# Kernel tuning notes

Measured on AMD Instinct MI355X. Metric: run time of the kernel, lower is better.

The kernel has to match this reference:

```python
import jax, jax.numpy as jnp
import numpy as np

QMIN, QMAX = -128, 127
EPS = float(np.finfo(np.float32).eps)


def _choose_qparams_and_quantize(x):
    # per-token asymmetric int8 qparams (token = all dims but last)
    mn = jnp.min(x, axis=-1, keepdims=True)
    mx = jnp.max(x, axis=-1, keepdims=True)
    mn = jnp.minimum(mn, 0.0)
    mx = jnp.maximum(mx, 0.0)
    scale = jnp.maximum((mx - mn) / float(QMAX - QMIN), EPS)
    d_min = mn / scale
    d_max = mx / scale
    zp = jnp.where((QMIN + d_min) + (QMAX + d_max) > 0, QMIN - d_min, QMAX - d_max)
    zp = jnp.round(jnp.clip(zp, QMIN, QMAX))
    q = jnp.clip(jnp.round(x / scale) + zp, QMIN, QMAX).astype(jnp.int8)
    return q, scale, zp.astype(jnp.int64)


def _dequant(q, scale, zp):
    return (q.astype(jnp.float32) - zp.astype(jnp.float32)) * scale


def setup_inputs() -> dict:
    key = jax.random.key(0)
    k1, k2 = jax.random.split(key)
    B, S, H, D = 1, 8192, 32, 128
    Snew = 128
    return {
        "input_pos": jnp.arange(Snew, dtype=jnp.int64),
        "k_val": jax.random.normal(k1, (B, Snew, H, D), dtype=jnp.float32),
        "v_val": jax.random.normal(k2, (B, Snew, H, D), dtype=jnp.float32),
        "k_cache": jnp.zeros((B, S, H, D), dtype=jnp.int8),
        "v_cache": jnp.zeros((B, S, H, D), dtype=jnp.int8),
        "k_cache_scales": jnp.ones((B, S, H, 1), dtype=jnp.float32),
        "v_cache_scales": jnp.ones((B, S, H, 1), dtype=jnp.float32),
        "k_cache_zero_points": jnp.ones((B, S, H, 1), dtype=jnp.int64),
        "v_cache_zero_points": jnp.ones((B, S, H, 1), dtype=jnp.int64),
    }


def reference(input_pos, k_val, v_val, k_cache, v_cache,
              k_cache_scales, v_cache_scales,
              k_cache_zero_points, v_cache_zero_points):
    qk, ks, kzp = _choose_qparams_and_quantize(k_val)
    qv, vs, vzp = _choose_qparams_and_quantize(v_val)
    start = input_pos[0]
    zero = jnp.zeros((), dtype=start.dtype)
    idx = (zero, start, zero, zero)
    k_cache = jax.lax.dynamic_update_slice(k_cache, qk, idx)
    k_cache_scales = jax.lax.dynamic_update_slice(k_cache_scales, ks, idx)
    k_cache_zero_points = jax.lax.dynamic_update_slice(k_cache_zero_points, kzp, idx)
    v_cache = jax.lax.dynamic_update_slice(v_cache, qv, idx)
    v_cache_scales = jax.lax.dynamic_update_slice(v_cache_scales, vs, idx)
    v_cache_zero_points = jax.lax.dynamic_update_slice(v_cache_zero_points, vzp, idx)
    k_out = _dequant(k_cache, k_cache_scales, k_cache_zero_points)
    v_out = _dequant(v_cache, v_cache_scales, v_cache_zero_points)
    return (k_out, v_out)
```

## Files before the change

kernel.cpp:

```cpp
#include <hip/hip_runtime.h>

constexpr int S = 8192, Snew = 128, H = 32, D = 128;
constexpr float QMINf = -128.0f, QMAXf = 127.0f;
constexpr float EPSf = 1.1920928955078125e-07f;

__global__ __launch_bounds__(256) void quant_update(
    const float* __restrict__ k_val, const float* __restrict__ v_val,
    const int* __restrict__ input_pos, float* __restrict__ out)
{
    const int gid  = blockIdx.x * 256 + threadIdx.x;
    const int wave = gid >> 6;
    const int lane = gid & 63;
    constexpr int TOK = Snew * H;
    if (wave >= 2 * TOK) return;
    const int tensor = wave >= TOK;
    const int tok    = tensor ? wave - TOK : wave;
    const float* src = tensor ? v_val : k_val;

    long long start = input_pos[0];
    if (start < 0) start = 0;
    if (start > (long long)(S - Snew)) start = S - Snew;

    const float2 x = ((const float2*)(src + (size_t)tok * D))[lane];
    float mn = fminf(x.x, x.y), mx = fmaxf(x.x, x.y);
    #pragma unroll
    for (int off = 1; off < 64; off <<= 1) {
        mn = fminf(mn, __shfl_xor(mn, off, 64));
        mx = fmaxf(mx, __shfl_xor(mx, off, 64));
    }
    mn = fminf(mn, 0.0f);
    mx = fmaxf(mx, 0.0f);
    const float scale = fmaxf((mx - mn) / 255.0f, EPSf);
    const float dmin = mn / scale;
    const float dmax = mx / scale;
    float zp = ((QMINf + dmin) + (QMAXf + dmax) > 0.0f) ? (QMINf - dmin)
                                                        : (QMAXf - dmax);
    zp = rintf(fminf(fmaxf(zp, QMINf), QMAXf));

    const float q0 = fminf(fmaxf(rintf(x.x / scale) + zp, QMINf), QMAXf);
    const float q1 = fminf(fmaxf(rintf(x.y / scale) + zp, QMINf), QMAXf);
    const float2 o = make_float2((q0 - zp) * scale, (q1 - zp) * scale);

    const int s_new = tok >> 5;
    const int h     = tok & (H - 1);
    const size_t off_el =
        ((size_t)tensor * S * H + (size_t)(start + s_new) * H + h) * (size_t)D;
    ((float2*)(out + off_el))[lane] = o;
}

__global__ __launch_bounds__(256) void dequant_cache(
    const int* __restrict__ k_cache, const int* __restrict__ v_cache,
    const float* __restrict__ k_scales, const float* __restrict__ v_scales,
    const int* __restrict__ k_zp, const int* __restrict__ v_zp,
    const int* __restrict__ input_pos, float* __restrict__ out)
{
    constexpr size_t TOK    = (size_t)S * H;
    constexpr size_t GROUPS = TOK * (D / 4);
    constexpr size_t TOTAL  = 2 * GROUPS;

    long long start = input_pos[0];
    if (start < 0) start = 0;
    if (start > (long long)(S - Snew)) start = S - Snew;
    const size_t s_lo = (size_t)start, s_hi = (size_t)start + Snew;

    const size_t stride = (size_t)gridDim.x * blockDim.x;
    for (size_t i = (size_t)blockIdx.x * blockDim.x + threadIdx.x;
         i < TOTAL; i += stride) {
        const size_t token  = i >> 5;
        const int    tensor = token >= TOK;
        const size_t tt     = tensor ? token - TOK : token;
        const size_t s      = tt >> 5;
        if (s >= s_lo && s < s_hi) continue;
        const size_t ig = tensor ? i - GROUPS : i;

        const int4  q4    = ((const int4*)(tensor ? v_cache : k_cache))[ig];
        const float scale = (tensor ? v_scales : k_scales)[tt];
        const float zp    = (float)(tensor ? v_zp : k_zp)[tt];

        float4 o;
        o.x = ((float)q4.x - zp) * scale;
        o.y = ((float)q4.y - zp) * scale;
        o.z = ((float)q4.z - zp) * scale;
        o.w = ((float)q4.w - zp) * scale;
        ((float4*)out)[i] = o;
    }
}

extern "C" void kernel_launch(void* const* d_in, const int* in_sizes, int n_in,
                              void* d_out, int out_size, void* d_ws, size_t ws_size,
                              hipStream_t stream) {
    (void)in_sizes; (void)n_in; (void)out_size; (void)d_ws; (void)ws_size;
    const int*   input_pos = (const int*)d_in[0];
    const float* k_val     = (const float*)d_in[1];
    const float* v_val     = (const float*)d_in[2];
    const int*   k_cache   = (const int*)d_in[3];
    const int*   v_cache   = (const int*)d_in[4];
    const float* k_scales  = (const float*)d_in[5];
    const float* v_scales  = (const float*)d_in[6];
    const int*   k_zp      = (const int*)d_in[7];
    const int*   v_zp      = (const int*)d_in[8];
    float*       out       = (float*)d_out;

    dequant_cache<<<2048, 256, 0, stream>>>(k_cache, v_cache,
                                            k_scales, v_scales,
                                            k_zp, v_zp, input_pos, out);
    quant_update<<<(2 * Snew * H * 64) / 256, 256, 0, stream>>>(
        k_val, v_val, input_pos, out);
}
```

Before: 113.9 us.

## Fuse quantize-update and cache dequant into one kernel with nontemporal accesses

Merges the two launches into one kernel: each block first quantizes four new tokens for its tensor, then runs a fixed-trip, unrolled grid-stride dequant loop over the cache with 32-bit indexing and nontemporal loads and stores. The goal is to remove a kernel launch and its serialization, cut 64-bit index arithmetic, and keep streaming data out of the caches. In exchange, every cache group is now loaded even inside the overwritten window (only the store is masked), and correctness depends on the two parts writing disjoint regions of the output.

```diff
diff --git a/kernel.cpp b/kernel.cpp
--- a/kernel.cpp
+++ b/kernel.cpp
@@ -1,88 +1,85 @@
 #include <hip/hip_runtime.h>
 
 constexpr int S = 8192, Snew = 128, H = 32, D = 128;
+constexpr int TOKENS = S * H;
+constexpr int GROUPS = TOKENS * (D / 4);
+constexpr int BLOCKS_HALF = 1024;
+constexpr int THREADS_HALF = BLOCKS_HALF * 256;
+constexpr int ITERS = GROUPS / THREADS_HALF;
+constexpr int GROUPS_PER_S = H * (D / 4);
 constexpr float QMINf = -128.0f, QMAXf = 127.0f;
 constexpr float EPSf = 1.1920928955078125e-07f;
 
-__global__ __launch_bounds__(256) void quant_update(
+typedef int   i32x4 __attribute__((ext_vector_type(4)));
+typedef float f32x4 __attribute__((ext_vector_type(4)));
+
+__global__ __launch_bounds__(256) void fused_kv(
     const float* __restrict__ k_val, const float* __restrict__ v_val,
+    const int* __restrict__ k_cache, const int* __restrict__ v_cache,
+    const float* __restrict__ k_scales, const float* __restrict__ v_scales,
+    const int* __restrict__ k_zp, const int* __restrict__ v_zp,
     const int* __restrict__ input_pos, float* __restrict__ out)
 {
-    const int gid  = blockIdx.x * 256 + threadIdx.x;
-    const int wave = gid >> 6;
-    const int lane = gid & 63;
-    constexpr int TOK = Snew * H;
-    if (wave >= 2 * TOK) return;
-    const int tensor = wave >= TOK;
-    const int tok    = tensor ? wave - TOK : wave;
-    const float* src = tensor ? v_val : k_val;
+    const int b      = blockIdx.x;
+    const int tensor = (b >= BLOCKS_HALF);
+    const int bh     = tensor ? b - BLOCKS_HALF : b;
 
     long long start = input_pos[0];
     if (start < 0) start = 0;
     if (start > (long long)(S - Snew)) start = S - Snew;
 
-    const float2 x = ((const float2*)(src + (size_t)tok * D))[lane];
-    float mn = fminf(x.x, x.y), mx = fmaxf(x.x, x.y);
-    #pragma unroll
-    for (int off = 1; off < 64; off <<= 1) {
-        mn = fminf(mn, __shfl_xor(mn, off, 64));
-        mx = fmaxf(mx, __shfl_xor(mx, off, 64));
+    {
+        const int lane = threadIdx.x & 63;
+        const int wv   = threadIdx.x >> 6;
+        const int tok  = bh * 4 + wv;
+        const float* src = tensor ? v_val : k_val;
+        const float2 x = ((const float2*)(src + (size_t)tok * D))[lane];
+        float mn = fminf(x.x, x.y), mx = fmaxf(x.x, x.y);
+        #pragma unroll
+        for (int off = 1; off < 64; off <<= 1) {
+            mn = fminf(mn, __shfl_xor(mn, off, 64));
+            mx = fmaxf(mx, __shfl_xor(mx, off, 64));
+        }
+        mn = fminf(mn, 0.0f);
+        mx = fmaxf(mx, 0.0f);
+        const float scale = fmaxf((mx - mn) / 255.0f, EPSf);
+        const float dmin = mn / scale, dmax = mx / scale;
+        float zp = ((QMINf + dmin) + (QMAXf + dmax) > 0.0f) ? (QMINf - dmin)
+                                                            : (QMAXf - dmax);
+        zp = rintf(fminf(fmaxf(zp, QMINf), QMAXf));
+        const float q0 = fminf(fmaxf(rintf(x.x / scale) + zp, QMINf), QMAXf);
+        const float q1 = fminf(fmaxf(rintf(x.y / scale) + zp, QMINf), QMAXf);
+        const int s_new = tok >> 5;
+        const int h     = tok & (H - 1);
+        const size_t off_el =
+            ((size_t)tensor * TOKENS + (size_t)(start + s_new) * H + h) * (size_t)D;
+        ((float2*)(out + off_el))[lane] =
+            make_float2((q0 - zp) * scale, (q1 - zp) * scale);
     }
-    mn = fminf(mn, 0.0f);
-    mx = fmaxf(mx, 0.0f);
-    const float scale = fmaxf((mx - mn) / 255.0f, EPSf);
-    const float dmin = mn / scale;
-    const float dmax = mx / scale;
-    float zp = ((QMINf + dmin) + (QMAXf + dmax) > 0.0f) ? (QMINf - dmin)
-                                                        : (QMAXf - dmax);
-    zp = rintf(fminf(fmaxf(zp, QMINf), QMAXf));
 
-    const float q0 = fminf(fmaxf(rintf(x.x / scale) + zp, QMINf), QMAXf);
-    const float q1 = fminf(fmaxf(rintf(x.y / scale) + zp, QMINf), QMAXf);
-    const float2 o = make_float2((q0 - zp) * scale, (q1 - zp) * scale);
+    const i32x4* __restrict__ c4  = (const i32x4*)(tensor ? v_cache : k_cache);
+    const float* __restrict__ scl = tensor ? v_scales : k_scales;
+    const int*   __restrict__ zps = tensor ? v_zp : k_zp;
+    f32x4* __restrict__ o4 = (f32x4*)out + (size_t)tensor * GROUPS;
 
-    const int s_new = tok >> 5;
-    const int h     = tok & (H - 1);
-    const size_t off_el =
-        ((size_t)tensor * S * H + (size_t)(start + s_new) * H + h) * (size_t)D;
-    ((float2*)(out + off_el))[lane] = o;
-}
+    const unsigned g_lo  = (unsigned)start * GROUPS_PER_S;
+    const unsigned g_len = (unsigned)Snew * GROUPS_PER_S;
 
-__global__ __launch_bounds__(256) void dequant_cache(
-    const int* __restrict__ k_cache, const int* __restrict__ v_cache,
-    const float* __restrict__ k_scales, const float* __restrict__ v_scales,
-    const int* __restrict__ k_zp, const int* __restrict__ v_zp,
-    const int* __restrict__ input_pos, float* __restrict__ out)
-{
-    constexpr size_t TOK    = (size_t)S * H;
-    constexpr size_t GROUPS = TOK * (D / 4);
-    constexpr size_t TOTAL  = 2 * GROUPS;
-
-    long long start = input_pos[0];
-    if (start < 0) start = 0;
-    if (start > (long long)(S - Snew)) start = S - Snew;
-    const size_t s_lo = (size_t)start, s_hi = (size_t)start + Snew;
-
-    const size_t stride = (size_t)gridDim.x * blockDim.x;
-    for (size_t i = (size_t)blockIdx.x * blockDim.x + threadIdx.x;
-         i < TOTAL; i += stride) {
-        const size_t token  = i >> 5;
-        const int    tensor = token >= TOK;
-        const size_t tt     = tensor ? token - TOK : token;
-        const size_t s      = tt >> 5;
-        if (s >= s_lo && s < s_hi) continue;
-        const size_t ig = tensor ? i - GROUPS : i;
-
-        const int4  q4    = ((const int4*)(tensor ? v_cache : k_cache))[ig];
-        const float scale = (tensor ? v_scales : k_scales)[tt];
-        const float zp    = (float)(tensor ? v_zp : k_zp)[tt];
-
-        float4 o;
+    const int tid = bh * 256 + (int)threadIdx.x;
+    #pragma unroll 8
+    for (int it = 0; it < ITERS; ++it) {
+        const int i     = tid + it * THREADS_HALF;
+        const int token = i >> 5;
+        const i32x4 q4    = __builtin_nontemporal_load(c4 + i);
+        const float scale = scl[token];
+        const float zp    = (float)zps[token];
+        f32x4 o;
         o.x = ((float)q4.x - zp) * scale;
         o.y = ((float)q4.y - zp) * scale;
         o.z = ((float)q4.z - zp) * scale;
         o.w = ((float)q4.w - zp) * scale;
-        ((float4*)out)[i] = o;
+        if ((unsigned)i - g_lo >= g_len)
+            __builtin_nontemporal_store(o, o4 + i);
     }
 }
 
@@ -101,9 +98,7 @@
     const int*   v_zp      = (const int*)d_in[8];
     float*       out       = (float*)d_out;
 
-    dequant_cache<<<2048, 256, 0, stream>>>(k_cache, v_cache,
-                                            k_scales, v_scales,
-                                            k_zp, v_zp, input_pos, out);
-    quant_update<<<(2 * Snew * H * 64) / 256, 256, 0, stream>>>(
-        k_val, v_val, input_pos, out);
+    fused_kv<<<2 * BLOCKS_HALF, 256, 0, stream>>>(
+        k_val, v_val, k_cache, v_cache, k_scales, v_scales,
+        k_zp, v_zp, input_pos, out);
 }
```

Measured after the change: 98.44 us (median of 2 runs). 13.6% less time.
